# Kernel tuning notes

Hardware: AMD Instinct MI355X
Metric: run time of the kernel (lower is better)

Reference implementation:

```python
import math
import jax, jax.numpy as jnp
import numpy as np

H, D = 16, 128
INNER = H * D
QUERY_DIM = 2048
EPS = 1e-6
NUM_SEQ_SHIFTS = 16
MAX_SEQ_LEN = 2048
CHANNEL_SHIFTS = [1, 2, 4, 8]


def compute_seq_shifts(num_shifts, max_len=2048):
    if num_shifts <= 1:
        return [0]
    half = (num_shifts - 1 + 1) // 2
    max_s = max(max_len // 2, 2)
    if half <= 1:
        positive = [1]
    else:
        positive = sorted(set(max(1, round(math.exp(math.log(max_s) * i / (half - 1)))) for i in range(half)))
        while len(positive) < half:
            new_vals = []
            for i in range(len(positive) - 1):
                mid = (positive[i] + positive[i + 1]) // 2
                if mid not in positive and mid not in new_vals:
                    new_vals.append(mid)
                if len(positive) + len(new_vals) >= half:
                    break
            if not new_vals:
                v = positive[-1] + 1
                while len(positive) + len(new_vals) < half and v <= max_s:
                    new_vals.append(v)
                    v += 1
            positive = sorted(set(positive + new_vals))[:half]
    shifts = [0]
    for s in positive:
        shifts.append(s)
        shifts.append(-s)
    return shifts[:num_shifts]

SEQ_SHIFTS = compute_seq_shifts(NUM_SEQ_SHIFTS, MAX_SEQ_LEN)


def setup_inputs() -> dict:
    key = jax.random.key(0)
    ks = jax.random.split(key, 12)
    s = 0.02
    return {
        "x": jax.random.normal(ks[0], (2, 2048, QUERY_DIM), dtype=jnp.float32),
        "wq": jax.random.normal(ks[1], (INNER, QUERY_DIM), dtype=jnp.float32) * s,
        "bq": jnp.zeros((INNER,), jnp.float32),
        "wk": jax.random.normal(ks[2], (INNER, QUERY_DIM), dtype=jnp.float32) * s,
        "bk": jnp.zeros((INNER,), jnp.float32),
        "wv": jax.random.normal(ks[3], (INNER, QUERY_DIM), dtype=jnp.float32) * s,
        "bv": jnp.zeros((INNER,), jnp.float32),
        "gq": jnp.ones((INNER,), jnp.float32),
        "gk": jnp.ones((INNER,), jnp.float32),
        "w_mix": jax.random.normal(ks[4], (1, 1 + len(CHANNEL_SHIFTS)), dtype=jnp.float32) * 0.4,
        "wo": jax.random.normal(ks[5], (QUERY_DIM, INNER), dtype=jnp.float32) * s,
        "bo": jnp.zeros((QUERY_DIM,), jnp.float32),
    }


def _rmsnorm(x, g, eps=EPS):
    return x * jax.lax.rsqrt(jnp.mean(x * x, axis=-1, keepdims=True) + eps) * g


def reference(x, wq, bq, wk, bk, wv, bv, gq, gk, w_mix, wo, bo):
    B, L, _ = x.shape
    scale = D ** (-0.5)
    q = _rmsnorm(x @ wq.T + bq, gq).reshape(B, L, H, D)
    k = _rmsnorm(x @ wk.T + bk, gk).reshape(B, L, H, D)
    v = (x @ wv.T + bv).reshape(B, L, H, D)
    # rolled gather indices: roll(k, s, axis=1)[l] == k[(l - s) % L]
    shifts = np.asarray(SEQ_SHIFTS)  # [S]
    idx = (np.arange(L)[None, :] - shifts[:, None]) % L  # [S, L]
    k_sh = k[:, idx]  # [B, S, L, H, D]
    v_sh = v[:, idx]  # [B, S, L, H, D]
    # channel-shifted q variants: [base, roll 1, 2, 4, 8] along D
    q_all = jnp.stack([q] + [jnp.roll(q, c, axis=-1) for c in CHANNEL_SHIFTS], axis=0)  # [C, B, L, H, D]
    scores = jnp.einsum('cblhd,bslhd->blhsc', q_all, k_sh) * scale  # [B, L, H, S, C]
    mixed = jnp.einsum('blhsc,c->blhs', scores, w_mix[0])  # score_mix Linear(C,1,bias=False)
    attn = jax.nn.softmax(mixed, axis=-1)  # softmax over shifts
    out = jnp.einsum('blhs,bslhd->blhd', attn, v_sh).reshape(B, L, H * D)
    return out @ wo.T + bo
```

## Files before the change

### kernel.cpp

```cpp
#include <hip/hip_runtime.h>
#include <hip/hip_bf16.h>
#include <stdint.h>

typedef __attribute__((ext_vector_type(8))) short v8s;
typedef __attribute__((ext_vector_type(8))) __bf16 bf16x8;
typedef __attribute__((ext_vector_type(4))) float v4f;

__device__ __forceinline__ unsigned short f2bf(float f) {
  unsigned int u = __float_as_uint(f);
  u += 0x7fff + ((u >> 16) & 1);
  return (unsigned short)(u >> 16);
}
__device__ __forceinline__ float bf2f(unsigned short h) {
  return __uint_as_float(((unsigned int)h) << 16);
}

__global__ void cast_main(const float* __restrict__ x,  const float* __restrict__ wq,
                          const float* __restrict__ wk, const float* __restrict__ wv,
                          unsigned short* __restrict__ xb, unsigned short* __restrict__ wqkvb) {
  const size_t MK = 8388608, NK = 4194304;
  size_t i = ((size_t)blockIdx.x * 256 + threadIdx.x) * 4;
  const float* s; unsigned short* d; size_t off;
  if (i < MK)               { s = x;  d = xb;              off = i; }
  else if (i < MK + NK)     { s = wq; d = wqkvb;           off = i - MK; }
  else if (i < MK + 2 * NK) { s = wk; d = wqkvb + NK;      off = i - MK - NK; }
  else                      { s = wv; d = wqkvb + 2 * NK;  off = i - MK - 2 * NK; }
  float4 v = *(const float4*)(s + off);
  ushort4 o;
  o.x = f2bf(v.x); o.y = f2bf(v.y); o.z = f2bf(v.z); o.w = f2bf(v.w);
  *(ushort4*)(d + off) = o;
}

__global__ void cast_f32_bf16(const float* __restrict__ s, unsigned short* __restrict__ d, int n) {
  int i = (blockIdx.x * blockDim.x + threadIdx.x) * 4;
  if (i >= n) return;
  float4 v = *(const float4*)(s + i);
  ushort4 o;
  o.x = f2bf(v.x); o.y = f2bf(v.y); o.z = f2bf(v.z); o.w = f2bf(v.w);
  *(ushort4*)(d + i) = o;
}

#define BM 128
#define BN 128
#define BK 64

__device__ __forceinline__ void gload_lds16(const void* g, void* l) {
  __builtin_amdgcn_global_load_lds(
      (const __attribute__((address_space(1))) void*)g,
      (__attribute__((address_space(3))) void*)l,
      16, 0, 0);
}

template <int OUT>
__global__ __launch_bounds__(256, 2) void gemm_bt(
    const unsigned short* __restrict__ A,
    const unsigned short* __restrict__ B,
    const float* __restrict__ bias0,
    const float* __restrict__ bias1,
    const float* __restrict__ bias2,
    void* __restrict__ D0, void* __restrict__ D1, void* __restrict__ D2,
    int K)
{
  __shared__ __align__(16) unsigned short As[BM * BK];
  __shared__ __align__(16) unsigned short Bs[BN * BK];

  const int tid  = threadIdx.x;
  const int lane = tid & 63;
  const int wid  = tid >> 6;
  const int wr   = wid >> 1, wc = wid & 1;

  const int tm = blockIdx.y * BM;
  const int tn = blockIdx.x * BN;

  const int srow = lane >> 3;
  const int scb  = lane & 7;
  const int gco  = (scb ^ srow) * 8;

  v4f acc[4][4];
#pragma unroll
  for (int m = 0; m < 4; ++m)
#pragma unroll
    for (int n = 0; n < 4; ++n)
      acc[m][n] = (v4f){0.f, 0.f, 0.f, 0.f};

  const unsigned short* Ab = A + (size_t)tm * K;
  const unsigned short* Bb = B + (size_t)tn * K;
  const int kTiles = K / BK;

  for (int kt = 0; kt < kTiles; ++kt) {
    const int k0 = kt * BK;
#pragma unroll
    for (int i = 0; i < 4; ++i) {
      const int r0 = wid * 32 + i * 8;
      gload_lds16(Ab + (size_t)(r0 + srow) * K + k0 + gco, &As[r0 * BK]);
    }
#pragma unroll
    for (int i = 0; i < 4; ++i) {
      const int r0 = wid * 32 + i * 8;
      gload_lds16(Bb + (size_t)(r0 + srow) * K + k0 + gco, &Bs[r0 * BK]);
    }
    __syncthreads();

#pragma unroll
    for (int ks = 0; ks < 2; ++ks) {
      bf16x8 av[4], bv[4];
#pragma unroll
      for (int m = 0; m < 4; ++m) {
        const int row  = wr * 64 + m * 16 + (lane & 15);
        const int cl   = ks * 4 + (lane >> 4);
        av[m] = *(const bf16x8*)&As[row * BK + ((cl ^ (row & 7)) * 8)];
      }
#pragma unroll
      for (int n = 0; n < 4; ++n) {
        const int row  = wc * 64 + n * 16 + (lane & 15);
        const int cl   = ks * 4 + (lane >> 4);
        bv[n] = *(const bf16x8*)&Bs[row * BK + ((cl ^ (row & 7)) * 8)];
      }
#pragma unroll
      for (int m = 0; m < 4; ++m)
#pragma unroll
        for (int n = 0; n < 4; ++n)
          acc[m][n] = __builtin_amdgcn_mfma_f32_16x16x32_bf16(av[m], bv[n], acc[m][n], 0, 0, 0);
    }
    __syncthreads();
  }

  const int cr0 = tm + wr * 64 + (lane >> 4) * 4;
  const int cc0 = tn + wc * 64 + (lane & 15);

  if (OUT == 0) {
    float* Dp = (float*)D0;
#pragma unroll
    for (int n = 0; n < 4; ++n) {
      const int col = cc0 + n * 16;
      const float bz = bias0[col];
#pragma unroll
      for (int m = 0; m < 4; ++m) {
#pragma unroll
        for (int r = 0; r < 4; ++r) {
          const int rr = cr0 + m * 16 + r;
          Dp[(size_t)rr * 2048 + col] = acc[m][n][r] + bz;
        }
      }
    }
  } else {
    const int sid = tn >> 11;
    const float* bp = (sid == 0) ? bias0 : (sid == 1) ? bias1 : bias2;
    unsigned short* Dq = (unsigned short*)((sid == 0) ? D0 : (sid == 1) ? D1 : D2);
#pragma unroll
    for (int n = 0; n < 4; ++n) {
      const int col = cc0 + n * 16;
      const int c2 = col & 2047;
      const float bz = bp[c2];
#pragma unroll
      for (int m = 0; m < 4; ++m) {
#pragma unroll
        for (int r = 0; r < 4; ++r) {
          const int rr = cr0 + m * 16 + r;
          const float val = acc[m][n][r] + bz;
          if (sid < 2) {
            Dq[(size_t)rr * 2048 + c2] = f2bf(val);
          } else {
            const int bb = rr >> 11, ll = rr & 2047;
            const int hh = c2 >> 7, dd = c2 & 127;
            Dq[(((size_t)(bb * 16 + hh)) * 2048 + ll) * 128 + dd] = f2bf(val);
          }
        }
      }
    }
  }
}

__global__ __launch_bounds__(256) void rmsnorm_mix(
    const unsigned short* __restrict__ Qb, const unsigned short* __restrict__ Kb,
    unsigned short* __restrict__ Qt, unsigned short* __restrict__ Kt,
    const float* __restrict__ gq, const float* __restrict__ gk,
    const float* __restrict__ wmix)
{
  const int row = blockIdx.x;
  const bool isQ = (blockIdx.y == 0);
  const unsigned short* src = (isQ ? Qb : Kb) + (size_t)row * 2048;
  unsigned short* dstbase = isQ ? Qt : Kt;
  const float* g = isQ ? gq : gk;
  const int b = row >> 11, l = row & 2047;

  __shared__ float sv[2048];
  __shared__ float red[4];

  const int t = threadIdx.x;
  v8s raw = *(const v8s*)(src + t * 8);
  float x[8];
  float ss = 0.f;
#pragma unroll
  for (int j = 0; j < 8; ++j) { x[j] = bf2f((unsigned short)raw[j]); ss += x[j] * x[j]; }
#pragma unroll
  for (int o = 32; o > 0; o >>= 1) ss += __shfl_xor(ss, o, 64);
  if ((t & 63) == 0) red[t >> 6] = ss;
  __syncthreads();
  const float tot = red[0] + red[1] + red[2] + red[3];
  const float inv = rsqrtf(tot * (1.0f / 2048.0f) + 1e-6f);

  const int h = t >> 4;
  unsigned short* dst = dstbase + (((size_t)(b * 16 + h)) * 2048 + l) * 128 + ((t * 8) & 127);

  if (isQ) {
#pragma unroll
    for (int j = 0; j < 8; ++j) sv[t * 8 + j] = x[j] * inv * g[t * 8 + j];
    __syncthreads();
    const float scale = 0.08838834764831845f;
    const float w0 = wmix[0], w1 = wmix[1], w2 = wmix[2], w3 = wmix[3], w4 = wmix[4];
    v8s ov;
#pragma unroll
    for (int j = 0; j < 8; ++j) {
      const int idx = t * 8 + j;
      const int hb = idx & ~127;
      const int d  = idx & 127;
      float a = w0 * sv[hb + d]
              + w1 * sv[hb + ((d - 1) & 127)]
              + w2 * sv[hb + ((d - 2) & 127)]
              + w3 * sv[hb + ((d - 4) & 127)]
              + w4 * sv[hb + ((d - 8) & 127)];
      ov[j] = (short)f2bf(a * scale);
    }
    *(v8s*)dst = ov;
  } else {
    v8s ov;
#pragma unroll
    for (int j = 0; j < 8; ++j) ov[j] = (short)f2bf(x[j] * inv * g[t * 8 + j]);
    *(v8s*)dst = ov;
  }
}

__global__ __launch_bounds__(512, 1) void attention_k(
    const unsigned short* __restrict__ Qt,
    const unsigned short* __restrict__ Kt,
    const unsigned short* __restrict__ Vt,
    unsigned short* __restrict__ AO)
{
  const int bid   = blockIdx.x;
  const int plane = bid & 31;
  const int ch    = bid >> 5;
  const int b = plane >> 4, h = plane & 15;
  const int l0 = ch * 128;
  const int w0 = (l0 + 2048 - 64) & 2047;

  __shared__ __align__(16) unsigned short Ks[256 * 128];
  __shared__ __align__(16) unsigned short Vs[256 * 128];
  __shared__ float sc[128][17];

  const int t    = threadIdx.x;
  const int lane = t & 63;
  const int w    = t >> 6;
  const int li   = t >> 2;
  const int q    = t & 3;
  const int myl  = l0 + li;

  const size_t pbase = (size_t)plane * (2048 * 128);

  {
    const int lr4 = lane >> 4;
    const int cp  = lane & 15;
#pragma unroll
    for (int j = 0; j < 8; ++j) {
      const int seg = w * 8 + j;
      const int rl  = seg * 4 + lr4;
      const int cl  = cp ^ (rl & 7);
      const int g   = (w0 + rl) & 2047;
      gload_lds16(Kt + pbase + (size_t)g * 128 + cl * 8, &Ks[seg * 512]);
      gload_lds16(Vt + pbase + (size_t)g * 128 + cl * 8, &Vs[seg * 512]);
    }
  }

  float qf[32];
  {
    const unsigned short* qp = Qt + pbase + (size_t)myl * 128 + q * 32;
#pragma unroll
    for (int i = 0; i < 4; ++i) {
      v8s qv = *(const v8s*)(qp + i * 8);
#pragma unroll
      for (int j = 0; j < 8; ++j) qf[i * 8 + j] = bf2f((unsigned short)qv[j]);
    }
  }

  asm volatile("s_waitcnt vmcnt(0)" ::: "memory");
  __syncthreads();

  const int SH[16] = {0, 1, -1, 3, -3, 7, -7, 20, -20, 53, -53, 141, -141, 380, -380, 1024};

#pragma unroll
  for (int s = 0; s < 16; ++s) {
    float dot = 0.f;
    if (s < 11) {
      const int rl = li + 64 - SH[s];
#pragma unroll
      for (int i = 0; i < 4; ++i) {
        v8s kv = *(const v8s*)&Ks[rl * 128 + (((q * 4 + i) ^ (rl & 7)) * 8)];
#pragma unroll
        for (int j = 0; j < 8; ++j) dot += qf[i * 8 + j] * bf2f((unsigned short)kv[j]);
      }
    } else {
      const int row = (myl - SH[s]) & 2047;
      const unsigned short* kp = Kt + pbase + (size_t)row * 128 + q * 32;
#pragma unroll
      for (int i = 0; i < 4; ++i) {
        v8s kv = *(const v8s*)(kp + i * 8);
#pragma unroll
        for (int j = 0; j < 8; ++j) dot += qf[i * 8 + j] * bf2f((unsigned short)kv[j]);
      }
    }
    dot += __shfl_xor(dot, 1, 64);
    dot += __shfl_xor(dot, 2, 64);
    if (q == 0) sc[li][s] = dot;
  }
  __syncthreads();

  {
    float v0[16];
#pragma unroll
    for (int s = 0; s < 16; ++s) v0[s] = sc[li][s];
    float mx = v0[0];
#pragma unroll
    for (int s = 1; s < 16; ++s) mx = fmaxf(mx, v0[s]);
    float sum = 0.f;
    float e[4];
#pragma unroll
    for (int s = 0; s < 16; ++s) {
      const float ee = __expf(v0[s] - mx);
      sum += ee;
      if ((s >> 2) == q) e[s & 3] = ee;
    }
    const float inv = 1.f / sum;
    __syncthreads();
#pragma unroll
    for (int i = 0; i < 4; ++i) sc[li][q * 4 + i] = e[i] * inv;
  }
  __syncthreads();

  float o[32];
#pragma unroll
  for (int i = 0; i < 32; ++i) o[i] = 0.f;
#pragma unroll
  for (int s = 0; s < 16; ++s) {
    const float p = sc[li][s];
    if (s < 11) {
      const int rl = li + 64 - SH[s];
#pragma unroll
      for (int i = 0; i < 4; ++i) {
        v8s vv = *(const v8s*)&Vs[rl * 128 + (((q * 4 + i) ^ (rl & 7)) * 8)];
#pragma unroll
        for (int j = 0; j < 8; ++j) o[i * 8 + j] += p * bf2f((unsigned short)vv[j]);
      }
    } else {
      const int row = (myl - SH[s]) & 2047;
      const unsigned short* vp = Vt + pbase + (size_t)row * 128 + q * 32;
#pragma unroll
      for (int i = 0; i < 4; ++i) {
        v8s vv = *(const v8s*)(vp + i * 8);
#pragma unroll
        for (int j = 0; j < 8; ++j) o[i * 8 + j] += p * bf2f((unsigned short)vv[j]);
      }
    }
  }

  unsigned short* op = AO + ((size_t)(b * 2048 + myl)) * 2048 + h * 128 + q * 32;
#pragma unroll
  for (int i = 0; i < 4; ++i) {
    v8s ov;
#pragma unroll
    for (int j = 0; j < 8; ++j) ov[j] = (short)f2bf(o[i * 8 + j]);
    *(v8s*)(op + i * 8) = ov;
  }
}

extern "C" void kernel_launch(void* const* d_in, const int* in_sizes, int n_in,
                              void* d_out, int out_size, void* d_ws, size_t ws_size,
                              hipStream_t stream) {
  const float* x    = (const float*)d_in[0];
  const float* wq   = (const float*)d_in[1];
  const float* bq   = (const float*)d_in[2];
  const float* wk   = (const float*)d_in[3];
  const float* bk   = (const float*)d_in[4];
  const float* wv   = (const float*)d_in[5];
  const float* bv   = (const float*)d_in[6];
  const float* gq   = (const float*)d_in[7];
  const float* gk   = (const float*)d_in[8];
  const float* wmix = (const float*)d_in[9];
  const float* wo   = (const float*)d_in[10];
  const float* bo   = (const float*)d_in[11];

  const int M = 4096;
  const int K = 2048;
  const int N = 2048;
  const size_t MB = 1024 * 1024;

  char* ws = (char*)d_ws;
  unsigned short* xb    = (unsigned short*)(ws + 0 * MB);
  unsigned short* Ktr   = (unsigned short*)(ws + 0 * MB);
  unsigned short* wqkvb = (unsigned short*)(ws + 16 * MB);
  unsigned short* wob   = (unsigned short*)(ws + 16 * MB);
  unsigned short* Qb    = (unsigned short*)(ws + 40 * MB);
  unsigned short* AOb   = (unsigned short*)(ws + 40 * MB);
  unsigned short* Kb    = (unsigned short*)(ws + 56 * MB);
  unsigned short* Vt    = (unsigned short*)(ws + 72 * MB);
  unsigned short* Qtr   = (unsigned short*)(ws + 88 * MB);

  cast_main<<<20480, 256, 0, stream>>>(x, wq, wk, wv, xb, wqkvb);

  gemm_bt<1><<<dim3(48, 32), 256, 0, stream>>>(xb, wqkvb, bq, bk, bv, Qb, Kb, Vt, K);

  cast_f32_bf16<<<(N * K) / 1024, 256, 0, stream>>>(wo, wob, N * K);

  rmsnorm_mix<<<dim3(M, 2), 256, 0, stream>>>(Qb, Kb, Qtr, Ktr, gq, gk, wmix);
  attention_k<<<512, 512, 0, stream>>>(Qtr, Ktr, Vt, AOb);

  gemm_bt<0><<<dim3(16, 32), 256, 0, stream>>>(AOb, wob, bo, nullptr, nullptr, d_out, nullptr, nullptr, K);
}
```

Baseline: 226.4 us.

## Add 256x256 pipelined QKV GEMM with XCD-aware tiling and fuse wo cast

```diff
diff --git a/kernel.cpp b/kernel.cpp
--- a/kernel.cpp
+++ b/kernel.cpp
@@ -15,51 +15,207 @@
   return __uint_as_float(((unsigned int)h) << 16);
 }
 
+#define LGKM0 asm volatile("s_waitcnt lgkmcnt(0)" ::: "memory")
+#define VMC4  asm volatile("s_waitcnt vmcnt(4)" ::: "memory")
+#define VMC0  asm volatile("s_waitcnt vmcnt(0)" ::: "memory")
+#define SCHEDB __builtin_amdgcn_sched_barrier(0)
+#define BAR __builtin_amdgcn_s_barrier()
+
+__device__ __forceinline__ void gload_lds16(const void* g, void* l) {
+  __builtin_amdgcn_global_load_lds(
+      (const __attribute__((address_space(1))) void*)g,
+      (__attribute__((address_space(3))) void*)l,
+      16, 0, 0);
+}
+
 __global__ void cast_main(const float* __restrict__ x,  const float* __restrict__ wq,
                           const float* __restrict__ wk, const float* __restrict__ wv,
-                          unsigned short* __restrict__ xb, unsigned short* __restrict__ wqkvb) {
+                          const float* __restrict__ wo,
+                          unsigned short* __restrict__ xb, unsigned short* __restrict__ wqkvb,
+                          unsigned short* __restrict__ wob) {
   const size_t MK = 8388608, NK = 4194304;
   size_t i = ((size_t)blockIdx.x * 256 + threadIdx.x) * 4;
   const float* s; unsigned short* d; size_t off;
   if (i < MK)               { s = x;  d = xb;              off = i; }
   else if (i < MK + NK)     { s = wq; d = wqkvb;           off = i - MK; }
   else if (i < MK + 2 * NK) { s = wk; d = wqkvb + NK;      off = i - MK - NK; }
-  else                      { s = wv; d = wqkvb + 2 * NK;  off = i - MK - 2 * NK; }
+  else if (i < MK + 3 * NK) { s = wv; d = wqkvb + 2 * NK;  off = i - MK - 2 * NK; }
+  else                      { s = wo; d = wob;             off = i - MK - 3 * NK; }
   float4 v = *(const float4*)(s + off);
   ushort4 o;
   o.x = f2bf(v.x); o.y = f2bf(v.y); o.z = f2bf(v.z); o.w = f2bf(v.w);
   *(ushort4*)(d + off) = o;
 }
 
-__global__ void cast_f32_bf16(const float* __restrict__ s, unsigned short* __restrict__ d, int n) {
-  int i = (blockIdx.x * blockDim.x + threadIdx.x) * 4;
-  if (i >= n) return;
-  float4 v = *(const float4*)(s + i);
-  ushort4 o;
-  o.x = f2bf(v.x); o.y = f2bf(v.y); o.z = f2bf(v.z); o.w = f2bf(v.w);
-  *(ushort4*)(d + i) = o;
+__global__ __launch_bounds__(512, 2) void gemm_qkv8(
+    const unsigned short* __restrict__ A,
+    const unsigned short* __restrict__ B,
+    const float* __restrict__ bias0, const float* __restrict__ bias1,
+    const float* __restrict__ bias2,
+    unsigned short* __restrict__ D0, unsigned short* __restrict__ D1,
+    unsigned short* __restrict__ D2, int K)
+{
+  __shared__ __align__(16) unsigned short As[2][2][128][64];
+  __shared__ __align__(16) unsigned short Bs[2][2][128][64];
+
+  const int bid = blockIdx.x;
+  const int xcd = bid & 7;
+  const int r   = bid >> 3;
+  const int by  = r / 3;
+  const int bx  = xcd * 3 + (r % 3);
+  const int tm  = by * 256;
+  const int tn  = bx * 256;
+
+  const int tid  = threadIdx.x;
+  const int lane = tid & 63;
+  const int wid  = tid >> 6;
+  const int wm   = wid >> 2;
+  const int wn   = wid & 3;
+
+  const int srow = lane >> 3;
+  const int gco  = ((lane & 7) ^ srow) * 8;
+
+  const unsigned short* Ag = A + (size_t)tm * K;
+  const unsigned short* Bg = B + (size_t)tn * K;
+
+  v4f acc[8][4];
+#pragma unroll
+  for (int m = 0; m < 8; ++m)
+#pragma unroll
+    for (int n = 0; n < 4; ++n)
+      acc[m][n] = (v4f){0.f, 0.f, 0.f, 0.f};
+
+  bf16x8 av[2][2], bv[4][2];
+  const int nt = K / 64;
+
+#define STAGE_A8(buf, kt, hf)                                                   \
+  {                                                                             \
+    _Pragma("unroll")                                                           \
+    for (int j = 0; j < 2; ++j) {                                               \
+      const int r8 = (wid * 2 + j) * 8;                                         \
+      gload_lds16(Ag + (size_t)((hf) * 128 + r8 + srow) * K + (kt) * 64 + gco,  \
+                  &As[buf][hf][r8][0]);                                         \
+    }                                                                           \
+  }
+#define STAGE_B8(buf, kt, hf)                                                   \
+  {                                                                             \
+    _Pragma("unroll")                                                           \
+    for (int j = 0; j < 2; ++j) {                                               \
+      const int r8 = (wid * 2 + j) * 8;                                         \
+      gload_lds16(Bg + (size_t)((hf) * 128 + r8 + srow) * K + (kt) * 64 + gco,  \
+                  &Bs[buf][hf][r8][0]);                                         \
+    }                                                                           \
+  }
+
+#define PHASE8(buf, p, STAGE_STMT, WAIT_STMT)                                   \
+  {                                                                             \
+    if ((p) == 0) {                                                             \
+      _Pragma("unroll")                                                         \
+      for (int nf = 0; nf < 4; ++nf) {                                          \
+        const int row_ = wn * 64 + nf * 16 + (lane & 15);                       \
+        _Pragma("unroll")                                                       \
+        for (int ks = 0; ks < 2; ++ks)                                          \
+          bv[nf][ks] = *(const bf16x8*)&Bs[buf][row_ >> 7][row_ & 127]          \
+              [((ks * 4 + (lane >> 4)) ^ (lane & 7)) * 8];                      \
+      }                                                                         \
+    }                                                                           \
+    _Pragma("unroll")                                                           \
+    for (int mf = 0; mf < 2; ++mf) {                                            \
+      const int rr_ = (p) * 32 + mf * 16 + (lane & 15);                         \
+      _Pragma("unroll")                                                         \
+      for (int ks = 0; ks < 2; ++ks)                                            \
+        av[mf][ks] = *(const bf16x8*)&As[buf][wm][rr_]                          \
+            [((ks * 4 + (lane >> 4)) ^ (lane & 7)) * 8];                        \
+    }                                                                           \
+    STAGE_STMT;                                                                 \
+    BAR;                                                                        \
+    LGKM0;                                                                      \
+    SCHEDB;                                                                     \
+    __builtin_amdgcn_s_setprio(1);                                              \
+    _Pragma("unroll")                                                           \
+    for (int ks = 0; ks < 2; ++ks)                                              \
+      _Pragma("unroll")                                                         \
+      for (int mf = 0; mf < 2; ++mf)                                            \
+        _Pragma("unroll")                                                       \
+        for (int nf = 0; nf < 4; ++nf)                                          \
+          acc[2 * (p) + mf][nf] = __builtin_amdgcn_mfma_f32_16x16x32_bf16(      \
+              av[mf][ks], bv[nf][ks], acc[2 * (p) + mf][nf], 0, 0, 0);          \
+    __builtin_amdgcn_s_setprio(0);                                              \
+    WAIT_STMT;                                                                  \
+    BAR;                                                                        \
+  }
+#define NOW8
+
+  STAGE_B8(0, 0, 0); STAGE_B8(0, 0, 1); STAGE_A8(0, 0, 0); STAGE_A8(0, 0, 1);
+  STAGE_B8(1, 1, 0); STAGE_B8(1, 1, 1);
+  VMC4;
+  BAR;
+
+  for (int i = 0; i < nt / 2 - 1; ++i) {
+    const int t1 = 2 * i + 1, t2 = 2 * i + 2, t3 = 2 * i + 3;
+    PHASE8(0, 0, STAGE_A8(1, t1, 0), NOW8);
+    PHASE8(0, 1, STAGE_A8(1, t1, 1), NOW8);
+    PHASE8(0, 2, STAGE_B8(0, t2, 0), NOW8);
+    PHASE8(0, 3, STAGE_B8(0, t2, 1), VMC4);
+    PHASE8(1, 0, STAGE_A8(0, t2, 0), NOW8);
+    PHASE8(1, 1, STAGE_A8(0, t2, 1), NOW8);
+    PHASE8(1, 2, STAGE_B8(1, t3, 0), NOW8);
+    PHASE8(1, 3, STAGE_B8(1, t3, 1), VMC4);
+  }
+  {
+    const int t1 = nt - 1;
+    PHASE8(0, 0, STAGE_A8(1, t1, 0), NOW8);
+    PHASE8(0, 1, STAGE_A8(1, t1, 1), NOW8);
+    PHASE8(0, 2, NOW8, NOW8);
+    PHASE8(0, 3, NOW8, VMC0);
+    PHASE8(1, 0, NOW8, NOW8);
+    PHASE8(1, 1, NOW8, NOW8);
+    PHASE8(1, 2, NOW8, NOW8);
+    PHASE8(1, 3, NOW8, NOW8);
+  }
+
+#undef STAGE_A8
+#undef STAGE_B8
+#undef PHASE8
+#undef NOW8
+
+  const int rr0 = tm + wm * 128 + (lane >> 4) * 4;
+  const int cc0 = tn + wn * 64 + (lane & 15);
+  const int sid = tn >> 11;
+  const float* bp = (sid == 0) ? bias0 : (sid == 1) ? bias1 : bias2;
+  unsigned short* Dq = (sid == 0) ? D0 : (sid == 1) ? D1 : D2;
+#pragma unroll
+  for (int n = 0; n < 4; ++n) {
+    const int col = cc0 + n * 16;
+    const int c2 = col & 2047;
+    const float bz = bp[c2];
+#pragma unroll
+    for (int m = 0; m < 8; ++m) {
+#pragma unroll
+      for (int rg = 0; rg < 4; ++rg) {
+        const int rr = rr0 + m * 16 + rg;
+        const float val = acc[m][n][rg] + bz;
+        if (sid < 2) {
+          Dq[(size_t)rr * 2048 + c2] = f2bf(val);
+        } else {
+          const int bb = rr >> 11, ll = rr & 2047;
+          const int hh = c2 >> 7, dd = c2 & 127;
+          Dq[(((size_t)(bb * 16 + hh)) * 2048 + ll) * 128 + dd] = f2bf(val);
+        }
+      }
+    }
+  }
 }
 
 #define BM 128
 #define BN 128
 #define BK 64
 
-__device__ __forceinline__ void gload_lds16(const void* g, void* l) {
-  __builtin_amdgcn_global_load_lds(
-      (const __attribute__((address_space(1))) void*)g,
-      (__attribute__((address_space(3))) void*)l,
-      16, 0, 0);
-}
-
-template <int OUT>
 __global__ __launch_bounds__(256, 2) void gemm_bt(
     const unsigned short* __restrict__ A,
     const unsigned short* __restrict__ B,
     const float* __restrict__ bias0,
-    const float* __restrict__ bias1,
-    const float* __restrict__ bias2,
-    void* __restrict__ D0, void* __restrict__ D1, void* __restrict__ D2,
-    int K)
+    float* __restrict__ D0, int K)
 {
   __shared__ __align__(16) unsigned short As[BM * BK];
   __shared__ __align__(16) unsigned short Bs[BN * BK];
@@ -127,45 +283,16 @@
 
   const int cr0 = tm + wr * 64 + (lane >> 4) * 4;
   const int cc0 = tn + wc * 64 + (lane & 15);
-
-  if (OUT == 0) {
-    float* Dp = (float*)D0;
-#pragma unroll
-    for (int n = 0; n < 4; ++n) {
-      const int col = cc0 + n * 16;
-      const float bz = bias0[col];
-#pragma unroll
-      for (int m = 0; m < 4; ++m) {
-#pragma unroll
-        for (int r = 0; r < 4; ++r) {
-          const int rr = cr0 + m * 16 + r;
-          Dp[(size_t)rr * 2048 + col] = acc[m][n][r] + bz;
-        }
-      }
-    }
-  } else {
-    const int sid = tn >> 11;
-    const float* bp = (sid == 0) ? bias0 : (sid == 1) ? bias1 : bias2;
-    unsigned short* Dq = (unsigned short*)((sid == 0) ? D0 : (sid == 1) ? D1 : D2);
-#pragma unroll
-    for (int n = 0; n < 4; ++n) {
-      const int col = cc0 + n * 16;
-      const int c2 = col & 2047;
-      const float bz = bp[c2];
-#pragma unroll
-      for (int m = 0; m < 4; ++m) {
-#pragma unroll
-        for (int r = 0; r < 4; ++r) {
-          const int rr = cr0 + m * 16 + r;
-          const float val = acc[m][n][r] + bz;
-          if (sid < 2) {
-            Dq[(size_t)rr * 2048 + c2] = f2bf(val);
-          } else {
-            const int bb = rr >> 11, ll = rr & 2047;
-            const int hh = c2 >> 7, dd = c2 & 127;
-            Dq[(((size_t)(bb * 16 + hh)) * 2048 + ll) * 128 + dd] = f2bf(val);
-          }
-        }
+#pragma unroll
+  for (int n = 0; n < 4; ++n) {
+    const int col = cc0 + n * 16;
+    const float bz = bias0[col];
+#pragma unroll
+    for (int m = 0; m < 4; ++m) {
+#pragma unroll
+      for (int r = 0; r < 4; ++r) {
+        const int rr = cr0 + m * 16 + r;
+        D0[(size_t)rr * 2048 + col] = acc[m][n][r] + bz;
       }
     }
   }
@@ -390,28 +517,25 @@
 
   const int M = 4096;
   const int K = 2048;
-  const int N = 2048;
   const size_t MB = 1024 * 1024;
 
   char* ws = (char*)d_ws;
   unsigned short* xb    = (unsigned short*)(ws + 0 * MB);
   unsigned short* Ktr   = (unsigned short*)(ws + 0 * MB);
   unsigned short* wqkvb = (unsigned short*)(ws + 16 * MB);
-  unsigned short* wob   = (unsigned short*)(ws + 16 * MB);
   unsigned short* Qb    = (unsigned short*)(ws + 40 * MB);
   unsigned short* AOb   = (unsigned short*)(ws + 40 * MB);
   unsigned short* Kb    = (unsigned short*)(ws + 56 * MB);
   unsigned short* Vt    = (unsigned short*)(ws + 72 * MB);
   unsigned short* Qtr   = (unsigned short*)(ws + 88 * MB);
-
-  cast_main<<<20480, 256, 0, stream>>>(x, wq, wk, wv, xb, wqkvb);
-
-  gemm_bt<1><<<dim3(48, 32), 256, 0, stream>>>(xb, wqkvb, bq, bk, bv, Qb, Kb, Vt, K);
-
-  cast_f32_bf16<<<(N * K) / 1024, 256, 0, stream>>>(wo, wob, N * K);
+  unsigned short* wob   = (unsigned short*)(ws + 104 * MB);
+
+  cast_main<<<24576, 256, 0, stream>>>(x, wq, wk, wv, wo, xb, wqkvb, wob);
+
+  gemm_qkv8<<<384, 512, 0, stream>>>(xb, wqkvb, bq, bk, bv, Qb, Kb, Vt, K);
 
   rmsnorm_mix<<<dim3(M, 2), 256, 0, stream>>>(Qb, Kb, Qtr, Ktr, gq, gk, wmix);
   attention_k<<<512, 512, 0, stream>>>(Qtr, Ktr, Vt, AOb);
 
-  gemm_bt<0><<<dim3(16, 32), 256, 0, stream>>>(AOb, wob, bo, nullptr, nullptr, d_out, nullptr, nullptr, K);
-}
+  gemm_bt<<<dim3(16, 32), 256, 0, stream>>>(AOb, wob, bo, (float*)d_out, K);
+}
```

Measured after the change: 268.8 us. 18.8% more time.

## Share one LDS buffer for K and V in attention, fold wo cast into main cast

Applied to the files above, without the earlier changes.

```diff
diff --git a/kernel.cpp b/kernel.cpp
--- a/kernel.cpp
+++ b/kernel.cpp
@@ -15,41 +15,35 @@
   return __uint_as_float(((unsigned int)h) << 16);
 }
 
+__device__ __forceinline__ void gload_lds16(const void* g, void* l) {
+  __builtin_amdgcn_global_load_lds(
+      (const __attribute__((address_space(1))) void*)g,
+      (__attribute__((address_space(3))) void*)l,
+      16, 0, 0);
+}
+
 __global__ void cast_main(const float* __restrict__ x,  const float* __restrict__ wq,
                           const float* __restrict__ wk, const float* __restrict__ wv,
-                          unsigned short* __restrict__ xb, unsigned short* __restrict__ wqkvb) {
+                          const float* __restrict__ wo,
+                          unsigned short* __restrict__ xb, unsigned short* __restrict__ wqkvb,
+                          unsigned short* __restrict__ wob) {
   const size_t MK = 8388608, NK = 4194304;
   size_t i = ((size_t)blockIdx.x * 256 + threadIdx.x) * 4;
   const float* s; unsigned short* d; size_t off;
   if (i < MK)               { s = x;  d = xb;              off = i; }
   else if (i < MK + NK)     { s = wq; d = wqkvb;           off = i - MK; }
   else if (i < MK + 2 * NK) { s = wk; d = wqkvb + NK;      off = i - MK - NK; }
-  else                      { s = wv; d = wqkvb + 2 * NK;  off = i - MK - 2 * NK; }
+  else if (i < MK + 3 * NK) { s = wv; d = wqkvb + 2 * NK;  off = i - MK - 2 * NK; }
+  else                      { s = wo; d = wob;             off = i - MK - 3 * NK; }
   float4 v = *(const float4*)(s + off);
   ushort4 o;
   o.x = f2bf(v.x); o.y = f2bf(v.y); o.z = f2bf(v.z); o.w = f2bf(v.w);
   *(ushort4*)(d + off) = o;
 }
 
-__global__ void cast_f32_bf16(const float* __restrict__ s, unsigned short* __restrict__ d, int n) {
-  int i = (blockIdx.x * blockDim.x + threadIdx.x) * 4;
-  if (i >= n) return;
-  float4 v = *(const float4*)(s + i);
-  ushort4 o;
-  o.x = f2bf(v.x); o.y = f2bf(v.y); o.z = f2bf(v.z); o.w = f2bf(v.w);
-  *(ushort4*)(d + i) = o;
-}
-
 #define BM 128
 #define BN 128
 #define BK 64
-
-__device__ __forceinline__ void gload_lds16(const void* g, void* l) {
-  __builtin_amdgcn_global_load_lds(
-      (const __attribute__((address_space(1))) void*)g,
-      (__attribute__((address_space(3))) void*)l,
-      16, 0, 0);
-}
 
 template <int OUT>
 __global__ __launch_bounds__(256, 2) void gemm_bt(
@@ -231,7 +225,7 @@
   }
 }
 
-__global__ __launch_bounds__(512, 1) void attention_k(
+__global__ __launch_bounds__(512, 4) void attention_k(
     const unsigned short* __restrict__ Qt,
     const unsigned short* __restrict__ Kt,
     const unsigned short* __restrict__ Vt,
@@ -244,8 +238,7 @@
   const int l0 = ch * 128;
   const int w0 = (l0 + 2048 - 64) & 2047;
 
-  __shared__ __align__(16) unsigned short Ks[256 * 128];
-  __shared__ __align__(16) unsigned short Vs[256 * 128];
+  __shared__ __align__(16) unsigned short KVs[256 * 128];
   __shared__ float sc[128][17];
 
   const int t    = threadIdx.x;
@@ -257,18 +250,16 @@
 
   const size_t pbase = (size_t)plane * (2048 * 128);
 
-  {
-    const int lr4 = lane >> 4;
-    const int cp  = lane & 15;
-#pragma unroll
-    for (int j = 0; j < 8; ++j) {
-      const int seg = w * 8 + j;
-      const int rl  = seg * 4 + lr4;
-      const int cl  = cp ^ (rl & 7);
-      const int g   = (w0 + rl) & 2047;
-      gload_lds16(Kt + pbase + (size_t)g * 128 + cl * 8, &Ks[seg * 512]);
-      gload_lds16(Vt + pbase + (size_t)g * 128 + cl * 8, &Vs[seg * 512]);
-    }
+  const int lr4 = lane >> 4;
+  const int cp  = lane & 15;
+
+#pragma unroll
+  for (int j = 0; j < 8; ++j) {
+    const int seg = w * 8 + j;
+    const int rl  = seg * 4 + lr4;
+    const int cl  = cp ^ (rl & 7);
+    const int g   = (w0 + rl) & 2047;
+    gload_lds16(Kt + pbase + (size_t)g * 128 + cl * 8, &KVs[seg * 512]);
   }
 
   float qf[32];
@@ -294,7 +285,7 @@
       const int rl = li + 64 - SH[s];
 #pragma unroll
       for (int i = 0; i < 4; ++i) {
-        v8s kv = *(const v8s*)&Ks[rl * 128 + (((q * 4 + i) ^ (rl & 7)) * 8)];
+        v8s kv = *(const v8s*)&KVs[rl * 128 + (((q * 4 + i) ^ (rl & 7)) * 8)];
 #pragma unroll
         for (int j = 0; j < 8; ++j) dot += qf[i * 8 + j] * bf2f((unsigned short)kv[j]);
       }
@@ -313,6 +304,15 @@
     if (q == 0) sc[li][s] = dot;
   }
   __syncthreads();
+
+#pragma unroll
+  for (int j = 0; j < 8; ++j) {
+    const int seg = w * 8 + j;
+    const int rl  = seg * 4 + lr4;
+    const int cl  = cp ^ (rl & 7);
+    const int g   = (w0 + rl) & 2047;
+    gload_lds16(Vt + pbase + (size_t)g * 128 + cl * 8, &KVs[seg * 512]);
+  }
 
   {
     float v0[16];
@@ -334,6 +334,7 @@
 #pragma unroll
     for (int i = 0; i < 4; ++i) sc[li][q * 4 + i] = e[i] * inv;
   }
+  asm volatile("s_waitcnt vmcnt(0)" ::: "memory");
   __syncthreads();
 
   float o[32];
@@ -346,7 +347,7 @@
       const int rl = li + 64 - SH[s];
 #pragma unroll
       for (int i = 0; i < 4; ++i) {
-        v8s vv = *(const v8s*)&Vs[rl * 128 + (((q * 4 + i) ^ (rl & 7)) * 8)];
+        v8s vv = *(const v8s*)&KVs[rl * 128 + (((q * 4 + i) ^ (rl & 7)) * 8)];
 #pragma unroll
         for (int j = 0; j < 8; ++j) o[i * 8 + j] += p * bf2f((unsigned short)vv[j]);
       }
@@ -390,25 +391,22 @@
 
   const int M = 4096;
   const int K = 2048;
-  const int N = 2048;
   const size_t MB = 1024 * 1024;
 
   char* ws = (char*)d_ws;
   unsigned short* xb    = (unsigned short*)(ws + 0 * MB);
   unsigned short* Ktr   = (unsigned short*)(ws + 0 * MB);
   unsigned short* wqkvb = (unsigned short*)(ws + 16 * MB);
-  unsigned short* wob   = (unsigned short*)(ws + 16 * MB);
   unsigned short* Qb    = (unsigned short*)(ws + 40 * MB);
   unsigned short* AOb   = (unsigned short*)(ws + 40 * MB);
   unsigned short* Kb    = (unsigned short*)(ws + 56 * MB);
   unsigned short* Vt    = (unsigned short*)(ws + 72 * MB);
   unsigned short* Qtr   = (unsigned short*)(ws + 88 * MB);
-
-  cast_main<<<20480, 256, 0, stream>>>(x, wq, wk, wv, xb, wqkvb);
+  unsigned short* wob   = (unsigned short*)(ws + 104 * MB);
+
+  cast_main<<<24576, 256, 0, stream>>>(x, wq, wk, wv, wo, xb, wqkvb, wob);
 
   gemm_bt<1><<<dim3(48, 32), 256, 0, stream>>>(xb, wqkvb, bq, bk, bv, Qb, Kb, Vt, K);
-
-  cast_f32_bf16<<<(N * K) / 1024, 256, 0, stream>>>(wo, wob, N * K);
 
   rmsnorm_mix<<<dim3(M, 2), 256, 0, stream>>>(Qb, Kb, Qtr, Ktr, gq, gk, wmix);
   attention_k<<<512, 512, 0, stream>>>(Qtr, Ktr, Vt, AOb);
```

Result: slower. 365.3 us (+61.4%).
